# Performance work log

Hardware: AMD Instinct MI355X
Metric: run time of the kernel (lower is better)

## Reference

```python
import jax, jax.numpy as jnp
import numpy as np

N, E, B, H, DE, L, V, NB, MAXNB, T, DEPTH = 30000, 60000, 256, 256, 256, 32, 40, 4, 6, 6, 4
PT, PA, PB = 1536, 1280, 2560


def mlp2(x, w1, b1, w2, b2):
    return jax.nn.relu(x @ w1 + b1) @ w2 + b2


def setup_inputs() -> dict:
    key = jax.random.key(0)
    ks = iter(jax.random.split(key, 64))
    nrm = lambda shape, s: jax.random.normal(next(ks), shape, jnp.float32) * s
    ri = lambda shape, hi: jax.random.randint(next(ks), shape, 0, hi, dtype=jnp.int32)
    zeros = lambda shape: jnp.zeros(shape, jnp.float32)
    inp = {}
    inp["src_graph_vecs"] = nrm((B, L), 1.0)
    inp["fnode"] = nrm((N, DE), 1.0)
    inp["fmess"] = nrm((E, DE), 1.0)
    # message-passing encoder params (GraphEncoder/rnn_cell surrogate)
    inp["W_h"] = nrm((DE, H), 0.05)
    inp["U_h"] = nrm((H, H), 0.05)
    inp["b_h"] = zeros((H,))
    inp["W_o"] = nrm((DE + H, H), 0.05)
    inp["b_o"] = zeros((H,))
    # topoNN: Linear(2H+L,H) ReLU Linear(H,1)
    inp["topo_w1"] = nrm((2 * H + L, H), 0.05); inp["topo_b1"] = zeros((H,))
    inp["topo_w2"] = nrm((H, 1), 0.05); inp["topo_b2"] = zeros((1,))
    # atomNN: Linear(2H+L,H) ReLU Linear(H,V)
    inp["atom_w1"] = nrm((2 * H + L, H), 0.05); inp["atom_b1"] = zeros((H,))
    inp["atom_w2"] = nrm((H, V), 0.05); inp["atom_b2"] = zeros((V,))
    # bondNN: Linear(3H+L,H) ReLU Linear(H,NB)
    inp["bond_w1"] = nrm((3 * H + L, H), 0.05); inp["bond_b1"] = zeros((H,))
    inp["bond_w2"] = nrm((H, NB), 0.05); inp["bond_b2"] = zeros((NB,))
    # R_bond: Linear(H+V,H)+ReLU ; W_bond: Linear(H+NB,H)+ReLU
    inp["rbond_w"] = nrm((H + V, H), 0.05); inp["rbond_b"] = zeros((H,))
    inp["wbond_w"] = nrm((H + NB, H), 0.05); inp["wbond_b"] = zeros((H,))
    # graph connectivity (padded neighbor lists; index 0 = padding message)
    inp["agraph"] = ri((N, MAXNB), E)
    inp["bgraph"] = ri((E, MAXNB), E)
    inp["node2graph"] = jnp.sort(ri((N,), B))
    inp["emask_steps"] = ri((T, E), 2)
    inp["vmask_steps"] = ri((T, N), 2)
    # flattened prediction lists (topo / atom / bond)
    inp["topo_step"] = ri((PT,), T); inp["topo_bid"] = ri((PT,), B)
    inp["topo_xid"] = ri((PT,), N); inp["topo_label"] = ri((PT,), 2)
    inp["atom_step"] = ri((PA,), T); inp["atom_bid"] = ri((PA,), B)
    inp["atom_xid"] = ri((PA,), N); inp["atom_label"] = ri((PA,), V)
    # bond preds come in groups of 2 sharing step/bid; hist accumulates within a group
    G = PB // 2
    inp["bond_step"] = jnp.repeat(ri((G,), T), 2)
    inp["bond_bid"] = jnp.repeat(ri((G,), B), 2)
    inp["bond_zid"] = ri((PB,), N)
    inp["bond_atom_type"] = ri((PB,), V)
    inp["bond_label"] = ri((PB,), NB)
    inp["bond_group_start"] = (jnp.arange(PB, dtype=jnp.int32) // 2) * 2
    return inp


def reference(src_graph_vecs, fnode, fmess, W_h, U_h, b_h, W_o, b_o,
              topo_w1, topo_b1, topo_w2, topo_b2,
              atom_w1, atom_b1, atom_w2, atom_b2,
              bond_w1, bond_b1, bond_w2, bond_b2,
              rbond_w, rbond_b, wbond_w, wbond_b,
              agraph, bgraph, node2graph, emask_steps, vmask_steps,
              topo_step, topo_bid, topo_xid, topo_label,
              atom_step, atom_bid, atom_xid, atom_label,
              bond_step, bond_bid, bond_zid, bond_atom_type, bond_label,
              bond_group_start):
    pad = (jnp.arange(E) > 0).astype(fmess.dtype)[:, None]  # message 0 is padding
    pre = fmess @ W_h  # [E,H], reused across steps/depth

    def encode(em, vm):
        # apply_graph_mask: zero out not-yet-revealed message indices
        ag = agraph * em[agraph]
        bg = bgraph * em[bgraph]
        h = jnp.zeros((E, H), fmess.dtype)
        for _ in range(DEPTH):
            nei = h[bg].sum(1)                         # [E,H] gather+sum over neighbors
            h = jax.nn.relu(pre + nei @ U_h + b_h) * pad
        node = jax.nn.relu(jnp.concatenate([fnode, h[ag].sum(1)], -1) @ W_o + b_o)
        return node * vm[:, None].astype(node.dtype)

    def step(c, ms):
        em, vm = ms
        return c, encode(em, vm)

    _, nodes = jax.lax.scan(step, 0, (emask_steps, vmask_steps))  # [T,N,H]
    gvec = jax.vmap(lambda n: jax.ops.segment_sum(n, node2graph, num_segments=B))(nodes)  # [T,B,H]

    E_a = jnp.eye(V, dtype=fnode.dtype)
    E_bm = jnp.eye(NB, dtype=fnode.dtype)

    # topo: BCEWithLogits (sum)
    tv = jnp.concatenate([gvec[topo_step, topo_bid], nodes[topo_step, topo_xid],
                          src_graph_vecs[topo_bid]], -1)
    tl = mlp2(tv, topo_w1, topo_b1, topo_w2, topo_b2)[:, 0]
    ty = topo_label.astype(tl.dtype)
    topo_loss = jnp.sum(jax.nn.softplus(tl) - tl * ty)

    # atom: CrossEntropy (sum)
    av = jnp.concatenate([gvec[atom_step, atom_bid], nodes[atom_step, atom_xid],
                          src_graph_vecs[atom_bid]], -1)
    al = mlp2(av, atom_w1, atom_b1, atom_w2, atom_b2)
    atom_loss = -jnp.sum(jnp.take_along_axis(jax.nn.log_softmax(al, -1), atom_label[:, None], 1))

    # bond: hist = within-group exclusive prefix sum of W_bond(node[z], onehot(bt)), only bt>0
    zn = nodes[bond_step, bond_zid]  # [PB,H]
    wb = jax.nn.relu(jnp.concatenate([zn, E_bm[bond_label]], -1) @ wbond_w + wbond_b)
    wb = wb * (bond_label > 0).astype(wb.dtype)[:, None]
    csum = jnp.cumsum(wb, 0)
    excl = csum - wb
    hist = excl - excl[bond_group_start]
    cur = jax.nn.relu(jnp.concatenate([hist, E_a[bond_atom_type]], -1) @ rbond_w + rbond_b)
    bv = jnp.concatenate([gvec[bond_step, bond_bid], cur, zn, src_graph_vecs[bond_bid]], -1)
    bl = mlp2(bv, bond_w1, bond_b1, bond_w2, bond_b2)
    bond_loss = -jnp.sum(jnp.take_along_axis(jax.nn.log_softmax(bl, -1), bond_label[:, None], 1))

    return (topo_loss + atom_loss + bond_loss) / B
```

## Files before the change

kernel.cpp:

```cpp
#include <hip/hip_runtime.h>
#include <cstdint>
#include <cstddef>

using short8  = __attribute__((ext_vector_type(8))) short;
using floatx4 = __attribute__((ext_vector_type(4))) float;
typedef unsigned short u16;

constexpr int NN = 30000;
constexpr int NE = 60000;
constexpr int BATCH = 256;
constexpr int VV = 40;
constexpr int NBOND = 4;
constexpr int TT = 6;
constexpr int PT = 1536, PA = 1280, PB = 2560;
constexpr int PALL = PT + PA + PB;

__device__ __forceinline__ float b2f(u16 h) {
  union { unsigned u; float f; } v; v.u = ((unsigned)h) << 16; return v.f;
}
__device__ __forceinline__ u16 f2b(float f) {
  union { float f; unsigned u; } v; v.f = f;
  unsigned r = v.u + 0x7FFFu + ((v.u >> 16) & 1u);
  return (u16)(r >> 16);
}
__device__ __forceinline__ float lo16(unsigned u) {
  union { unsigned x; float f; } v; v.x = u << 16; return v.f;
}
__device__ __forceinline__ float hi16(unsigned u) {
  union { unsigned x; float f; } v; v.x = u & 0xffff0000u; return v.f;
}
__device__ __forceinline__ unsigned pack2(float a, float b) {
  return ((unsigned)f2b(a)) | (((unsigned)f2b(b)) << 16);
}

template<int AMODE>
__global__ __launch_bounds__(512) void gemm_n256_kernel(
    const void* __restrict__ Av, int M,
    const u16* __restrict__ Bt,
    u16* __restrict__ C, const float* __restrict__ abias)
{
  __shared__ __align__(16) u16 As[128][40];
  __shared__ __align__(16) u16 Bs[256][40];
  const int tid = threadIdx.x;
  const int rowbase = blockIdx.x * 128;
  const int wave = tid >> 6, lane = tid & 63;
  const int wm = wave >> 2, wn = wave & 3;
  const int lr = lane & 15, lk = (lane >> 4) * 8;
  const int arow = tid >> 2, ac8 = (tid & 3) * 8;
  const int brow = tid >> 1, bc16 = (tid & 1) * 16;

  floatx4 acc[4][4];
#pragma unroll
  for (int i = 0; i < 4; i++)
#pragma unroll
    for (int j = 0; j < 4; j++) acc[i][j] = {0.f, 0.f, 0.f, 0.f};

  for (int k0 = 0; k0 < 256; k0 += 32) {
    {
      int grow = rowbase + arow;
      uint4 av = {0u, 0u, 0u, 0u};
      if (AMODE == 1) {
        if (grow < M) {
          const float* Af = (const float*)Av;
          float4 f0 = *(const float4*)(Af + (long)grow * 256 + k0 + ac8);
          float4 f1 = *(const float4*)(Af + (long)grow * 256 + k0 + ac8 + 4);
          av.x = pack2(f0.x, f0.y); av.y = pack2(f0.z, f0.w);
          av.z = pack2(f1.x, f1.y); av.w = pack2(f1.z, f1.w);
        }
      } else {
        if (grow < M) av = *(const uint4*)((const u16*)Av + (long)grow * 256 + k0 + ac8);
        if (AMODE == 2) {
          if (grow == 0) { av = {0u, 0u, 0u, 0u}; }
          else {
            float4 b0 = *(const float4*)(abias + k0 + ac8);
            float4 b1 = *(const float4*)(abias + k0 + ac8 + 4);
            float a0 = fmaxf(lo16(av.x) + b0.x, 0.f), a1 = fmaxf(hi16(av.x) + b0.y, 0.f);
            float a2 = fmaxf(lo16(av.y) + b0.z, 0.f), a3 = fmaxf(hi16(av.y) + b0.w, 0.f);
            float a4 = fmaxf(lo16(av.z) + b1.x, 0.f), a5 = fmaxf(hi16(av.z) + b1.y, 0.f);
            float a6 = fmaxf(lo16(av.w) + b1.z, 0.f), a7 = fmaxf(hi16(av.w) + b1.w, 0.f);
            av.x = pack2(a0, a1); av.y = pack2(a2, a3);
            av.z = pack2(a4, a5); av.w = pack2(a6, a7);
          }
        }
      }
      *(uint4*)(&As[arow][ac8]) = av;
      uint4 v0 = *(const uint4*)(Bt + (long)brow * 256 + k0 + bc16);
      uint4 v1 = *(const uint4*)(Bt + (long)brow * 256 + k0 + bc16 + 8);
      *(uint4*)(&Bs[brow][bc16]) = v0;
      *(uint4*)(&Bs[brow][bc16 + 8]) = v1;
    }
    __syncthreads();
    short8 af[4], bf[4];
#pragma unroll
    for (int mt = 0; mt < 4; mt++) af[mt] = *(const short8*)(&As[wm * 64 + mt * 16 + lr][lk]);
#pragma unroll
    for (int nt = 0; nt < 4; nt++) bf[nt] = *(const short8*)(&Bs[wn * 64 + nt * 16 + lr][lk]);
#pragma unroll
    for (int mt = 0; mt < 4; mt++)
#pragma unroll
      for (int nt = 0; nt < 4; nt++)
        acc[mt][nt] = __builtin_amdgcn_mfma_f32_16x16x32_bf16(af[mt], bf[nt], acc[mt][nt], 0, 0, 0);
    __syncthreads();
  }

  const int rq = (lane >> 4) * 4;
#pragma unroll
  for (int mt = 0; mt < 4; mt++) {
#pragma unroll
    for (int nt = 0; nt < 4; nt++) {
      int gcol = wn * 64 + nt * 16 + lr;
#pragma unroll
      for (int r2 = 0; r2 < 4; r2++) {
        int grow = rowbase + wm * 64 + mt * 16 + rq + r2;
        if (grow < M) C[(long)grow * 256 + gcol] = f2b(acc[mt][nt][r2]);
      }
    }
  }
}

template<int MODE>
__global__ __launch_bounds__(256) void gemm_bt_kernel(
    const u16* __restrict__ A, int lda, int M,
    const u16* __restrict__ Bt, int K,
    u16* __restrict__ C, int ldc, const float* __restrict__ bias)
{
  __shared__ __align__(16) u16 As[128][56];
  __shared__ __align__(16) u16 Bs[128][56];
  const int tid  = threadIdx.x;
  const int wave = tid >> 6, lane = tid & 63;
  const int wm = wave >> 1, wn = wave & 1;
  const int lr = lane & 15, lk = (lane >> 4) * 8;
  const int rowbase = blockIdx.x * 128;
  const int colbase = blockIdx.y * 128;

  floatx4 acc[4][4];
#pragma unroll
  for (int i = 0; i < 4; i++)
#pragma unroll
    for (int j = 0; j < 4; j++) acc[i][j] = {0.f, 0.f, 0.f, 0.f};

  for (int k0 = 0; k0 < K; k0 += 32) {
#pragma unroll
    for (int r = 0; r < 2; r++) {
      int c = tid + 256 * r;
      int row = c >> 2, cc = (c & 3) * 8;
      int grow = rowbase + row;
      uint4 av = {0u, 0u, 0u, 0u};
      if (grow < M) av = *(const uint4*)(A + (long)grow * lda + k0 + cc);
      *(uint4*)(&As[row][cc]) = av;
      uint4 bv = *(const uint4*)(Bt + (long)(colbase + row) * K + k0 + cc);
      *(uint4*)(&Bs[row][cc]) = bv;
    }
    __syncthreads();
    short8 af[4], bf[4];
#pragma unroll
    for (int mt = 0; mt < 4; mt++) af[mt] = *(const short8*)(&As[wm * 64 + mt * 16 + lr][lk]);
#pragma unroll
    for (int nt = 0; nt < 4; nt++) bf[nt] = *(const short8*)(&Bs[wn * 64 + nt * 16 + lr][lk]);
#pragma unroll
    for (int mt = 0; mt < 4; mt++)
#pragma unroll
      for (int nt = 0; nt < 4; nt++)
        acc[mt][nt] = __builtin_amdgcn_mfma_f32_16x16x32_bf16(af[mt], bf[nt], acc[mt][nt], 0, 0, 0);
    __syncthreads();
  }

  const int rq = (lane >> 4) * 4;
#pragma unroll
  for (int mt = 0; mt < 4; mt++) {
#pragma unroll
    for (int nt = 0; nt < 4; nt++) {
      int gcol = colbase + wn * 64 + nt * 16 + lr;
#pragma unroll
      for (int r2 = 0; r2 < 4; r2++) {
        int grow = rowbase + wm * 64 + mt * 16 + rq + r2;
        if (grow < M) {
          float v = acc[mt][nt][r2];
          if (MODE == 1) { v += bias[gcol]; v = v > 0.f ? v : 0.f; }
          C[(long)grow * ldc + gcol] = f2b(v);
        }
      }
    }
  }
}

__global__ __launch_bounds__(256) void gemm_ta_kernel(
    const u16* __restrict__ A,
    const u16* __restrict__ Bt1, const u16* __restrict__ Bt2,
    const float* __restrict__ b1, const float* __restrict__ b2,
    u16* __restrict__ C)
{
  constexpr int K = 544;
  __shared__ __align__(16) u16 As[128][56];
  __shared__ __align__(16) u16 Bs[128][56];
  const int tid  = threadIdx.x;
  const int wave = tid >> 6, lane = tid & 63;
  const int wm = wave >> 1, wn = wave & 1;
  const int lr = lane & 15, lk = (lane >> 4) * 8;
  const int rowbase = blockIdx.x * 128;
  const int colbase = blockIdx.y * 128;
  const u16* Bt = (rowbase < PT) ? Bt1 : Bt2;
  const float* bias = (rowbase < PT) ? b1 : b2;

  floatx4 acc[4][4];
#pragma unroll
  for (int i = 0; i < 4; i++)
#pragma unroll
    for (int j = 0; j < 4; j++) acc[i][j] = {0.f, 0.f, 0.f, 0.f};

  for (int k0 = 0; k0 < K; k0 += 32) {
#pragma unroll
    for (int r = 0; r < 2; r++) {
      int c = tid + 256 * r;
      int row = c >> 2, cc = (c & 3) * 8;
      int grow = rowbase + row;
      uint4 av = *(const uint4*)(A + (long)grow * K + k0 + cc);
      *(uint4*)(&As[row][cc]) = av;
      uint4 bv = *(const uint4*)(Bt + (long)(colbase + row) * K + k0 + cc);
      *(uint4*)(&Bs[row][cc]) = bv;
    }
    __syncthreads();
    short8 af[4], bf[4];
#pragma unroll
    for (int mt = 0; mt < 4; mt++) af[mt] = *(const short8*)(&As[wm * 64 + mt * 16 + lr][lk]);
#pragma unroll
    for (int nt = 0; nt < 4; nt++) bf[nt] = *(const short8*)(&Bs[wn * 64 + nt * 16 + lr][lk]);
#pragma unroll
    for (int mt = 0; mt < 4; mt++)
#pragma unroll
      for (int nt = 0; nt < 4; nt++)
        acc[mt][nt] = __builtin_amdgcn_mfma_f32_16x16x32_bf16(af[mt], bf[nt], acc[mt][nt], 0, 0, 0);
    __syncthreads();
  }

  const int rq = (lane >> 4) * 4;
#pragma unroll
  for (int mt = 0; mt < 4; mt++) {
#pragma unroll
    for (int nt = 0; nt < 4; nt++) {
      int gcol = colbase + wn * 64 + nt * 16 + lr;
#pragma unroll
      for (int r2 = 0; r2 < 4; r2++) {
        int grow = rowbase + wm * 64 + mt * 16 + rq + r2;
        float v = acc[mt][nt][r2] + bias[gcol];
        v = v > 0.f ? v : 0.f;
        C[(long)grow * 256 + gcol] = f2b(v);
      }
    }
  }
}

__global__ __launch_bounds__(256) void gemm_logits_kernel(
    const u16* __restrict__ A, const u16* __restrict__ w2c,
    const float* __restrict__ b2c, float* __restrict__ L)
{
  __shared__ __align__(16) u16 As[128][40];
  __shared__ __align__(16) u16 Bs[64][40];
  const int tid = threadIdx.x;
  const int rowbase = blockIdx.x * 128;
  const int seg = (rowbase < PT) ? 0 : (rowbase < PT + PA ? 1 : 2);
  const u16* Bt = w2c + seg * 64 * 256;
  const int wave = tid >> 6, lane = tid & 63;
  const int wm = wave >> 1, wn = wave & 1;
  const int lr = lane & 15, lk = (lane >> 4) * 8;
  const int sr = tid >> 2, sc = (tid & 3) * 8;

  floatx4 acc[4][2];
#pragma unroll
  for (int i = 0; i < 4; i++)
#pragma unroll
    for (int j = 0; j < 2; j++) acc[i][j] = {0.f, 0.f, 0.f, 0.f};

  for (int k0 = 0; k0 < 256; k0 += 32) {
    *(uint4*)(&As[sr][sc]) = *(const uint4*)(A + (long)(rowbase + sr) * 256 + k0 + sc);
    *(uint4*)(&As[sr + 64][sc]) = *(const uint4*)(A + (long)(rowbase + sr + 64) * 256 + k0 + sc);
    *(uint4*)(&Bs[sr][sc]) = *(const uint4*)(Bt + (long)sr * 256 + k0 + sc);
    __syncthreads();
    short8 af[4], bf[2];
#pragma unroll
    for (int mt = 0; mt < 4; mt++) af[mt] = *(const short8*)(&As[wm * 64 + mt * 16 + lr][lk]);
#pragma unroll
    for (int nt = 0; nt < 2; nt++) bf[nt] = *(const short8*)(&Bs[wn * 32 + nt * 16 + lr][lk]);
#pragma unroll
    for (int mt = 0; mt < 4; mt++)
#pragma unroll
      for (int nt = 0; nt < 2; nt++)
        acc[mt][nt] = __builtin_amdgcn_mfma_f32_16x16x32_bf16(af[mt], bf[nt], acc[mt][nt], 0, 0, 0);
    __syncthreads();
  }

  const int rq = (lane >> 4) * 4;
#pragma unroll
  for (int mt = 0; mt < 4; mt++) {
#pragma unroll
    for (int nt = 0; nt < 2; nt++) {
      int gcol = wn * 32 + nt * 16 + lr;
#pragma unroll
      for (int r2 = 0; r2 < 4; r2++) {
        int grow = rowbase + wm * 64 + mt * 16 + rq + r2;
        L[(long)grow * 64 + gcol] = acc[mt][nt][r2] + b2c[seg * 64 + gcol];
      }
    }
  }
}

__global__ __launch_bounds__(256) void build_w2c_kernel(
    const float* __restrict__ tw2, const float* __restrict__ tb2,
    const float* __restrict__ aw2, const float* __restrict__ ab2,
    const float* __restrict__ bw2, const float* __restrict__ bb2,
    u16* __restrict__ w2c, float* __restrict__ b2c)
{
  int idx = blockIdx.x * 256 + threadIdx.x;
  int seg = idx / 16384;
  int rem = idx - seg * 16384;
  int n = rem >> 8, k = rem & 255;
  const float* W; const float* B; int NC;
  if (seg == 0)      { W = tw2; B = tb2; NC = 1; }
  else if (seg == 1) { W = aw2; B = ab2; NC = VV; }
  else               { W = bw2; B = bb2; NC = NBOND; }
  w2c[idx] = (n < NC) ? f2b(W[(long)k * NC + n]) : (u16)0;
  if (idx < 192) {
    int s2 = idx / 64, n2 = idx & 63;
    const float* B2 = (s2 == 0) ? tb2 : (s2 == 1 ? ab2 : bb2);
    int NC2 = (s2 == 0) ? 1 : (s2 == 1 ? VV : NBOND);
    b2c[idx] = (n2 < NC2) ? B2[n2] : 0.f;
  }
}

__global__ __launch_bounds__(256) void loss_finalize_kernel(
    const float* __restrict__ L,
    const int* __restrict__ tlab, const int* __restrict__ alab,
    const int* __restrict__ blab, float* __restrict__ out)
{
  __shared__ float part[4];
  int wave = threadIdx.x >> 6, lane = threadIdx.x & 63;
  int r = blockIdx.x * 4 + wave;
  float contrib = 0.f;
  if (r < PT) {
    float l = L[(long)r * 64];
    float y = (float)tlab[r];
    contrib = fmaxf(l, 0.f) + log1pf(expf(-fabsf(l))) - l * y;
  } else {
    int NC, lb;
    if (r < PT + PA) { NC = VV; lb = alab[r - PT]; }
    else             { NC = NBOND; lb = blab[r - PT - PA]; }
    bool valid = lane < NC;
    float logit = valid ? L[(long)r * 64 + lane] : -1e30f;
    float m = logit;
#pragma unroll
    for (int off = 32; off > 0; off >>= 1) m = fmaxf(m, __shfl_xor(m, off));
    float e = valid ? expf(logit - m) : 0.f;
#pragma unroll
    for (int off = 32; off > 0; off >>= 1) e += __shfl_xor(e, off);
    float lse = m + logf(e);
    float ll = __shfl(logit, lb);
    contrib = lse - ll;
  }
  if (lane == 0) part[wave] = contrib;
  __syncthreads();
  if (threadIdx.x == 0)
    atomicAdd(out, (part[0] + part[1] + part[2] + part[3]) * (1.0f / BATCH));
}

template<int SHARED_TAB>
__global__ __launch_bounds__(256) void gather_e2_kernel(
    const u16* __restrict__ tab, const u16* __restrict__ pre,
    const int* __restrict__ bgraph, const int* __restrict__ emask,
    const float* __restrict__ bias, int t0, u16* __restrict__ G)
{
  int r0 = blockIdx.x * 8;
  int tl = r0 / NE;
  int e0 = r0 - tl * NE;
  const int* em_t = emask + (long)(t0 + tl) * NE;
  __shared__ int sidx[8][6];
  int tid = threadIdx.x;
  if (tid < 48) {
    int rr = tid / 6, j = tid - rr * 6;
    int v = bgraph[(long)(e0 + rr) * 6 + j];
    v = v * em_t[v];
    sidx[rr][j] = SHARED_TAB ? v : (tl * NE + v);
  }
  __syncthreads();
  int rl = tid >> 5, ch = (tid & 31) * 8;
  int e = e0 + rl;
  uint4 p = *(const uint4*)(pre + (long)e * 256 + ch);
  float a0 = lo16(p.x), a1 = hi16(p.x), a2 = lo16(p.y), a3 = hi16(p.y);
  float a4 = lo16(p.z), a5 = hi16(p.z), a6 = lo16(p.w), a7 = hi16(p.w);
#pragma unroll
  for (int j = 0; j < 6; j++) {
    uint4 g = *(const uint4*)(tab + (long)sidx[rl][j] * 256 + ch);
    a0 += lo16(g.x); a1 += hi16(g.x); a2 += lo16(g.y); a3 += hi16(g.y);
    a4 += lo16(g.z); a5 += hi16(g.z); a6 += lo16(g.w); a7 += hi16(g.w);
  }
  float4 b0 = *(const float4*)(bias + ch);
  float4 b1 = *(const float4*)(bias + ch + 4);
  a0 += b0.x; a1 += b0.y; a2 += b0.z; a3 += b0.w;
  a4 += b1.x; a5 += b1.y; a6 += b1.z; a7 += b1.w;
  if (e == 0) { a0 = a1 = a2 = a3 = a4 = a5 = a6 = a7 = 0.f; }
  else {
    a0 = fmaxf(a0, 0.f); a1 = fmaxf(a1, 0.f); a2 = fmaxf(a2, 0.f); a3 = fmaxf(a3, 0.f);
    a4 = fmaxf(a4, 0.f); a5 = fmaxf(a5, 0.f); a6 = fmaxf(a6, 0.f); a7 = fmaxf(a7, 0.f);
  }
  uint4 o; o.x = pack2(a0, a1); o.y = pack2(a2, a3); o.z = pack2(a4, a5); o.w = pack2(a6, a7);
  *(uint4*)(G + (long)(r0 + rl) * 256 + ch) = o;
}

__global__ __launch_bounds__(256) void gather_n2_kernel(
    const u16* __restrict__ tab, const u16* __restrict__ fo,
    const int* __restrict__ agraph, const int* __restrict__ emask,
    const float* __restrict__ bias, const int* __restrict__ vmask,
    int t0, u16* __restrict__ node)
{
  int r0 = blockIdx.x * 8;
  int tl = r0 / NN;
  int n0 = r0 - tl * NN;
  const int* em_t = emask + (long)(t0 + tl) * NE;
  const int* vm_t = vmask + (long)(t0 + tl) * NN;
  __shared__ int sidx[8][6];
  __shared__ int svm[8];
  int tid = threadIdx.x;
  if (tid < 48) {
    int rr = tid / 6, j = tid - rr * 6;
    int v = agraph[(long)(n0 + rr) * 6 + j];
    sidx[rr][j] = tl * NE + v * em_t[v];
  }
  if (tid >= 48 && tid < 56) svm[tid - 48] = vm_t[n0 + (tid - 48)];
  __syncthreads();
  int rl = tid >> 5, ch = (tid & 31) * 8;
  int n = n0 + rl;
  uint4 p = *(const uint4*)(fo + (long)n * 256 + ch);
  float a0 = lo16(p.x), a1 = hi16(p.x), a2 = lo16(p.y), a3 = hi16(p.y);
  float a4 = lo16(p.z), a5 = hi16(p.z), a6 = lo16(p.w), a7 = hi16(p.w);
#pragma unroll
  for (int j = 0; j < 6; j++) {
    uint4 g = *(const uint4*)(tab + (long)sidx[rl][j] * 256 + ch);
    a0 += lo16(g.x); a1 += hi16(g.x); a2 += lo16(g.y); a3 += hi16(g.y);
    a4 += lo16(g.z); a5 += hi16(g.z); a6 += lo16(g.w); a7 += hi16(g.w);
  }
  float4 b0 = *(const float4*)(bias + ch);
  float4 b1 = *(const float4*)(bias + ch + 4);
  a0 = fmaxf(a0 + b0.x, 0.f); a1 = fmaxf(a1 + b0.y, 0.f);
  a2 = fmaxf(a2 + b0.z, 0.f); a3 = fmaxf(a3 + b0.w, 0.f);
  a4 = fmaxf(a4 + b1.x, 0.f); a5 = fmaxf(a5 + b1.y, 0.f);
  a6 = fmaxf(a6 + b1.z, 0.f); a7 = fmaxf(a7 + b1.w, 0.f);
  if (svm[rl] == 0) { a0 = a1 = a2 = a3 = a4 = a5 = a6 = a7 = 0.f; }
  uint4 o; o.x = pack2(a0, a1); o.y = pack2(a2, a3); o.z = pack2(a4, a5); o.w = pack2(a6, a7);
  *(uint4*)(node + (long)(r0 + rl) * 256 + ch) = o;
}

__global__ __launch_bounds__(256) void init_zero_kernel(float* __restrict__ gv,
                                                        float* __restrict__ out)
{
  int i = blockIdx.x * 256 + threadIdx.x;
  gv[i] = 0.f;
  if (i == 0) out[0] = 0.f;
}

__global__ __launch_bounds__(256) void transpose_all_kernel(
    const float* W_h, const float* U_h, const float* W_o,
    const float* tw1, const float* aw1, const float* bw1,
    const float* rw, const float* ww,
    u16* Wh_t, u16* Uh_t, u16* Wo1_t, u16* Wo2_t,
    u16* tw1_t, u16* aw1_t, u16* bw1_t, u16* rw_t, u16* ww_t)
{
  int b = blockIdx.x;
  const float* W; int K, Kpad; u16* Bt; int base;
  if      (b < 256)  { W = W_h;  K = 256; Kpad = 256; Bt = Wh_t;  base = 0; }
  else if (b < 512)  { W = U_h;  K = 256; Kpad = 256; Bt = Uh_t;  base = 256; }
  else if (b < 768)  { W = W_o;  K = 256; Kpad = 256; Bt = Wo1_t; base = 512; }
  else if (b < 1024) { W = W_o + 256 * 256; K = 256; Kpad = 256; Bt = Wo2_t; base = 768; }
  else if (b < 1568) { W = tw1;  K = 544; Kpad = 544; Bt = tw1_t; base = 1024; }
  else if (b < 2112) { W = aw1;  K = 544; Kpad = 544; Bt = aw1_t; base = 1568; }
  else if (b < 2912) { W = bw1;  K = 800; Kpad = 800; Bt = bw1_t; base = 2112; }
  else if (b < 3232) { W = rw;   K = 296; Kpad = 320; Bt = rw_t;  base = 2912; }
  else               { W = ww;   K = 260; Kpad = 288; Bt = ww_t;  base = 3232; }
  int idx = (b - base) * 256 + threadIdx.x;
  int n = idx / Kpad, k = idx - n * Kpad;
  Bt[idx] = (k < K) ? f2b(W[(long)k * 256 + n]) : (u16)0;
}

__global__ __launch_bounds__(256) void gvec_head_kernel(int t0,
    const u16* __restrict__ node, const int* __restrict__ n2g,
    float* __restrict__ gv,
    const int* __restrict__ tstep, const int* __restrict__ txid,
    const int* __restrict__ astep, const int* __restrict__ axid,
    const int* __restrict__ bstep, const int* __restrict__ bzid,
    u16* __restrict__ tv, u16* __restrict__ av, u16* __restrict__ bv,
    u16* __restrict__ wbin)
{
  int b = blockIdx.x;
  if (b < 1876) {
    int tl = (b >= 938) ? 1 : 0;
    int r0 = (b - tl * 938) * 32;
    if (r0 >= NN) return;
    int h = threadIdx.x;
    const u16* nd = node + (long)tl * NN * 256;
    float* gb = gv + (long)(t0 + tl) * BATCH * 256;
    int rend = r0 + 32; if (rend > NN) rend = NN;
    int gprev = n2g[r0];
    float acc = 0.f;
    for (int r = r0; r < rend; r++) {
      int g = n2g[r];
      if (g != gprev) { atomicAdd(gb + gprev * 256 + h, acc); acc = 0.f; gprev = g; }
      acc += b2f(nd[(long)r * 256 + h]);
    }
    atomicAdd(gb + gprev * 256 + h, acc);
    return;
  }
  int wave = threadIdx.x >> 6, lane = threadIdx.x & 63;
  int r = (b - 1876) * 4 + wave;
  int c = lane * 4;
  if (r < PT) {
    int st = tstep[r];
    if (st < t0 || st >= t0 + 2) return;
    ushort4 v = *(const ushort4*)(node + ((long)(st - t0) * NN + txid[r]) * 256 + c);
    *(ushort4*)(tv + (long)r * 544 + 256 + c) = v;
  } else if (r < PT + PA) {
    int i = r - PT;
    int st = astep[i];
    if (st < t0 || st >= t0 + 2) return;
    ushort4 v = *(const ushort4*)(node + ((long)(st - t0) * NN + axid[i]) * 256 + c);
    *(ushort4*)(av + (long)i * 544 + 256 + c) = v;
  } else if (r < PALL) {
    int i = r - PT - PA;
    int st = bstep[i];
    if (st < t0 || st >= t0 + 2) return;
    ushort4 v = *(const ushort4*)(node + ((long)(st - t0) * NN + bzid[i]) * 256 + c);
    *(ushort4*)(bv + (long)i * 800 + 512 + c) = v;
    *(ushort4*)(wbin + (long)i * 288 + c) = v;
  }
}

__global__ __launch_bounds__(256) void build_static_kernel(
    const float* __restrict__ gvec, const float* __restrict__ src,
    const int* __restrict__ tstep, const int* __restrict__ tbid,
    const int* __restrict__ astep, const int* __restrict__ abid,
    const int* __restrict__ bstep, const int* __restrict__ bbid,
    const int* __restrict__ blabel, const int* __restrict__ batype,
    u16* __restrict__ tv, u16* __restrict__ av, u16* __restrict__ bv,
    u16* __restrict__ wbin, u16* __restrict__ rbin)
{
  int wave = threadIdx.x >> 6, lane = threadIdx.x & 63;
  int r = blockIdx.x * 4 + wave;
  int c = lane * 4;
  if (r < PT) {
    int st = tstep[r], bid = tbid[r];
    const float* g = gvec + ((long)st * BATCH + bid) * 256;
    u16* d = tv + (long)r * 544;
    float4 g4 = *(const float4*)(g + c);
    d[c] = f2b(g4.x); d[c + 1] = f2b(g4.y); d[c + 2] = f2b(g4.z); d[c + 3] = f2b(g4.w);
    if (lane < 8) {
      float4 s4 = *(const float4*)(src + bid * 32 + c);
      d[512 + c] = f2b(s4.x); d[512 + c + 1] = f2b(s4.y);
      d[512 + c + 2] = f2b(s4.z); d[512 + c + 3] = f2b(s4.w);
    }
  } else if (r < PT + PA) {
    int i = r - PT;
    int st = astep[i], bid = abid[i];
    const float* g = gvec + ((long)st * BATCH + bid) * 256;
    u16* d = av + (long)i * 544;
    float4 g4 = *(const float4*)(g + c);
    d[c] = f2b(g4.x); d[c + 1] = f2b(g4.y); d[c + 2] = f2b(g4.z); d[c + 3] = f2b(g4.w);
    if (lane < 8) {
      float4 s4 = *(const float4*)(src + bid * 32 + c);
      d[512 + c] = f2b(s4.x); d[512 + c + 1] = f2b(s4.y);
      d[512 + c + 2] = f2b(s4.z); d[512 + c + 3] = f2b(s4.w);
    }
  } else if (r < PALL) {
    int i = r - PT - PA;
    int st = bstep[i], bid = bbid[i];
    const float* g = gvec + ((long)st * BATCH + bid) * 256;
    u16* d = bv + (long)i * 800;
    float4 g4 = *(const float4*)(g + c);
    d[c] = f2b(g4.x); d[c + 1] = f2b(g4.y); d[c + 2] = f2b(g4.z); d[c + 3] = f2b(g4.w);
    if (lane < 8) {
      float4 s4 = *(const float4*)(src + bid * 32 + c);
      d[768 + c] = f2b(s4.x); d[768 + c + 1] = f2b(s4.y);
      d[768 + c + 2] = f2b(s4.z); d[768 + c + 3] = f2b(s4.w);
      int bl = blabel[i];
      u16* wd = wbin + (long)i * 288 + 256;
      for (int q = 0; q < 4; q++) {
        int k = c + q;
        wd[k] = f2b((k < NBOND && bl == k) ? 1.f : 0.f);
      }
    }
    if (lane < 16) {
      int at = batype[i];
      u16* rd = rbin + (long)i * 320 + 256;
      for (int q = 0; q < 4; q++) {
        int k = c + q;
        rd[k] = f2b((k < VV && at == k) ? 1.f : 0.f);
      }
    }
  }
}

__global__ __launch_bounds__(256) void hist_kernel(
    const u16* __restrict__ wb, const int* __restrict__ gs_arr,
    const int* __restrict__ blabel, u16* __restrict__ rbin)
{
  int wave = threadIdx.x >> 6, lane = threadIdx.x & 63;
  int r = blockIdx.x * 4 + wave;
  if (r >= PB) return;
  int c = lane * 4;
  float a0 = 0.f, a1 = 0.f, a2 = 0.f, a3 = 0.f;
  int gs = gs_arr[r];
  for (int j = gs; j < r; j++) {
    if (blabel[j] > 0) {
      ushort4 g = *(const ushort4*)(wb + (long)j * 256 + c);
      a0 += b2f(g.x); a1 += b2f(g.y); a2 += b2f(g.z); a3 += b2f(g.w);
    }
  }
  u16* rd = rbin + (long)r * 320;
  rd[c] = f2b(a0); rd[c + 1] = f2b(a1); rd[c + 2] = f2b(a2); rd[c + 3] = f2b(a3);
}

extern "C" void kernel_launch(void* const* d_in, const int* in_sizes, int n_in,
                              void* d_out, int out_size, void* d_ws, size_t ws_size,
                              hipStream_t stream)
{
  const float* src      = (const float*)d_in[0];
  const float* fnode    = (const float*)d_in[1];
  const float* fmess    = (const float*)d_in[2];
  const float* W_h      = (const float*)d_in[3];
  const float* U_h      = (const float*)d_in[4];
  const float* b_h      = (const float*)d_in[5];
  const float* W_o      = (const float*)d_in[6];
  const float* b_o      = (const float*)d_in[7];
  const float* topo_w1  = (const float*)d_in[8];
  const float* topo_b1  = (const float*)d_in[9];
  const float* topo_w2  = (const float*)d_in[10];
  const float* topo_b2  = (const float*)d_in[11];
  const float* atom_w1  = (const float*)d_in[12];
  const float* atom_b1  = (const float*)d_in[13];
  const float* atom_w2  = (const float*)d_in[14];
  const float* atom_b2  = (const float*)d_in[15];
  const float* bond_w1  = (const float*)d_in[16];
  const float* bond_b1  = (const float*)d_in[17];
  const float* bond_w2  = (const float*)d_in[18];
  const float* bond_b2  = (const float*)d_in[19];
  const float* rbond_w  = (const float*)d_in[20];
  const float* rbond_b  = (const float*)d_in[21];
  const float* wbond_w  = (const float*)d_in[22];
  const float* wbond_b  = (const float*)d_in[23];
  const int* agraph     = (const int*)d_in[24];
  const int* bgraph     = (const int*)d_in[25];
  const int* node2graph = (const int*)d_in[26];
  const int* emask      = (const int*)d_in[27];
  const int* vmask      = (const int*)d_in[28];
  const int* topo_step  = (const int*)d_in[29];
  const int* topo_bid   = (const int*)d_in[30];
  const int* topo_xid   = (const int*)d_in[31];
  const int* topo_label = (const int*)d_in[32];
  const int* atom_step  = (const int*)d_in[33];
  const int* atom_bid   = (const int*)d_in[34];
  const int* atom_xid   = (const int*)d_in[35];
  const int* atom_label = (const int*)d_in[36];
  const int* bond_step  = (const int*)d_in[37];
  const int* bond_bid   = (const int*)d_in[38];
  const int* bond_zid   = (const int*)d_in[39];
  const int* bond_atype = (const int*)d_in[40];
  const int* bond_label = (const int*)d_in[41];
  const int* bond_gs    = (const int*)d_in[42];

  char* wp = (char*)d_ws;
  auto alloc = [&](size_t bytes) -> char* {
    char* p = wp; wp += (bytes + 255) & ~(size_t)255; return p;
  };
  u16* preB    = (u16*)alloc((size_t)NE * 256 * 2);
  u16* hu1B    = (u16*)alloc((size_t)NE * 256 * 2);
  u16* foB     = (u16*)alloc((size_t)NN * 256 * 2);
  float* gvec  = (float*)alloc((size_t)TT * BATCH * 256 * 4);
  u16* Wh_t    = (u16*)alloc(256 * 256 * 2);
  u16* Uh_t    = (u16*)alloc(256 * 256 * 2);
  u16* Wo1_t   = (u16*)alloc(256 * 256 * 2);
  u16* Wo2_t   = (u16*)alloc(256 * 256 * 2);
  u16* tw1_t   = (u16*)alloc(256 * 544 * 2);
  u16* aw1_t   = (u16*)alloc(256 * 544 * 2);
  u16* bw1_t   = (u16*)alloc(256 * 800 * 2);
  u16* rw_t    = (u16*)alloc(256 * 320 * 2);
  u16* ww_t    = (u16*)alloc(256 * 288 * 2);
  u16* w2c     = (u16*)alloc(3 * 64 * 256 * 2);
  float* b2c   = (float*)alloc(192 * 4);
  u16* tva     = (u16*)alloc((size_t)(PT + PA) * 544 * 2);
  u16* bv      = (u16*)alloc((size_t)PB * 800 * 2);
  u16* wbin    = (u16*)alloc((size_t)PB * 288 * 2);
  u16* rbin    = (u16*)alloc((size_t)PB * 320 * 2);
  u16* wb      = (u16*)alloc((size_t)PB * 256 * 2);
  u16* hid_all = (u16*)alloc((size_t)PALL * 256 * 2);
  float* logitsL = (float*)alloc((size_t)PALL * 64 * 4);
  u16* G       = (u16*)alloc((size_t)2 * NE * 256 * 2);
  u16* T       = (u16*)alloc((size_t)2 * NE * 256 * 2);
  u16* tv      = tva;
  u16* av      = tva + (size_t)PT * 544;
  u16* nodeB   = G;

  float* out = (float*)d_out;

  init_zero_kernel<<<1536, 256, 0, stream>>>(gvec, out);
  transpose_all_kernel<<<3520, 256, 0, stream>>>(W_h, U_h, W_o, topo_w1, atom_w1, bond_w1,
      rbond_w, wbond_w, Wh_t, Uh_t, Wo1_t, Wo2_t, tw1_t, aw1_t, bw1_t, rw_t, ww_t);
  build_w2c_kernel<<<192, 256, 0, stream>>>(topo_w2, topo_b2, atom_w2, atom_b2,
                                            bond_w2, bond_b2, w2c, b2c);

  gemm_n256_kernel<1><<<(NE + 127) / 128, 512, 0, stream>>>(fmess, NE, Wh_t, preB, nullptr);
  gemm_n256_kernel<1><<<(NN + 127) / 128, 512, 0, stream>>>(fnode, NN, Wo1_t, foB, nullptr);
  gemm_n256_kernel<2><<<(NE + 127) / 128, 512, 0, stream>>>(preB, NE, Uh_t, hu1B, b_h);

  for (int t0 = 0; t0 < TT; t0 += 2) {
    int M2 = 2 * NE;
    int gb = 2 * NE / 8;
    int mb = (M2 + 127) / 128;
    gather_e2_kernel<1><<<gb, 256, 0, stream>>>(hu1B, preB, bgraph, emask, b_h, t0, G);
    gemm_n256_kernel<0><<<mb, 512, 0, stream>>>(G, M2, Uh_t, T, nullptr);
    gather_e2_kernel<0><<<gb, 256, 0, stream>>>(T, preB, bgraph, emask, b_h, t0, G);
    gemm_n256_kernel<0><<<mb, 512, 0, stream>>>(G, M2, Uh_t, T, nullptr);
    gather_e2_kernel<0><<<gb, 256, 0, stream>>>(T, preB, bgraph, emask, b_h, t0, G);
    gemm_n256_kernel<0><<<mb, 512, 0, stream>>>(G, M2, Wo2_t, T, nullptr);
    gather_n2_kernel<<<2 * NN / 8, 256, 0, stream>>>(T, foB, agraph, emask, b_o,
                                                     vmask, t0, nodeB);
    gvec_head_kernel<<<3220, 256, 0, stream>>>(t0, nodeB, node2graph, gvec,
        topo_step, topo_xid, atom_step, atom_xid, bond_step, bond_zid,
        tv, av, bv, wbin);
  }

  build_static_kernel<<<1344, 256, 0, stream>>>(gvec, src,
      topo_step, topo_bid, atom_step, atom_bid, bond_step, bond_bid,
      bond_label, bond_atype, tv, av, bv, wbin, rbin);

  gemm_ta_kernel<<<dim3((PT + PA) / 128, 2), 256, 0, stream>>>(tva, tw1_t, aw1_t,
                                                               topo_b1, atom_b1, hid_all);
  gemm_bt_kernel<1><<<dim3(20, 2), 256, 0, stream>>>(wbin, 288, PB, ww_t, 288,
                                                     wb, 256, wbond_b);
  hist_kernel<<<640, 256, 0, stream>>>(wb, bond_gs, bond_label, rbin);
  gemm_bt_kernel<1><<<dim3(20, 2), 256, 0, stream>>>(rbin, 320, PB, rw_t, 320,
                                                     bv + 256, 800, rbond_b);
  gemm_bt_kernel<1><<<dim3(20, 2), 256, 0, stream>>>(bv, 800, PB, bw1_t, 800,
                                                     hid_all + (size_t)(PT + PA) * 256,
                                                     256, bond_b1);

  gemm_logits_kernel<<<PALL / 128, 256, 0, stream>>>(hid_all, w2c, b2c, logitsL);
  loss_finalize_kernel<<<PALL / 4, 256, 0, stream>>>(logitsL, topo_label, atom_label,
                                                     bond_label, out);
}
```

Baseline: 1.140 ms.

## Store message-passing intermediates in FP8 to halve gather and GEMM traffic

The edge message tensors (pre-activations, hidden updates, gather outputs and GEMM outputs in the recurrent loop) are stored as FP8 bytes instead of bf16, with conversion to bf16 when loading GEMM A tiles and FP8 packing on output. This halves the memory traffic of the bandwidth-bound gather and GEMM passes over 120k-row buffers. nodeB gets its own buffer since G shrank. The trade-off is a large loss of precision in the recurrent message state, which may push the loss outside tolerance.

```diff
diff --git a/kernel.cpp b/kernel.cpp
--- a/kernel.cpp
+++ b/kernel.cpp
@@ -4,7 +4,9 @@
 
 using short8  = __attribute__((ext_vector_type(8))) short;
 using floatx4 = __attribute__((ext_vector_type(4))) float;
+using floatx2 = __attribute__((ext_vector_type(2))) float;
 typedef unsigned short u16;
+typedef unsigned char  u8;
 
 constexpr int NN = 30000;
 constexpr int NE = 60000;
@@ -32,12 +34,26 @@
 __device__ __forceinline__ unsigned pack2(float a, float b) {
   return ((unsigned)f2b(a)) | (((unsigned)f2b(b)) << 16);
 }
-
-template<int AMODE>
+__device__ __forceinline__ floatx2 f8lo(unsigned v) {
+  return __builtin_amdgcn_cvt_pk_f32_fp8((int)v, false);
+}
+__device__ __forceinline__ floatx2 f8hi(unsigned v) {
+  return __builtin_amdgcn_cvt_pk_f32_fp8((int)v, true);
+}
+__device__ __forceinline__ unsigned pk8(float a, float b, float c, float d) {
+  int w = __builtin_amdgcn_cvt_pk_fp8_f32(a, b, 0, false);
+  w = __builtin_amdgcn_cvt_pk_fp8_f32(c, d, w, true);
+  return (unsigned)w;
+}
+__device__ __forceinline__ u8 f2f8(float v) {
+  return (u8)(__builtin_amdgcn_cvt_pk_fp8_f32(v, v, 0, false) & 0xff);
+}
+
+template<int AMODE, int OMODE>
 __global__ __launch_bounds__(512) void gemm_n256_kernel(
     const void* __restrict__ Av, int M,
     const u16* __restrict__ Bt,
-    u16* __restrict__ C, const float* __restrict__ abias)
+    void* __restrict__ Cv, const float* __restrict__ abias)
 {
   __shared__ __align__(16) u16 As[128][40];
   __shared__ __align__(16) u16 Bs[256][40];
@@ -68,19 +84,25 @@
           av.z = pack2(f1.x, f1.y); av.w = pack2(f1.z, f1.w);
         }
       } else {
-        if (grow < M) av = *(const uint4*)((const u16*)Av + (long)grow * 256 + k0 + ac8);
-        if (AMODE == 2) {
-          if (grow == 0) { av = {0u, 0u, 0u, 0u}; }
-          else {
-            float4 b0 = *(const float4*)(abias + k0 + ac8);
-            float4 b1 = *(const float4*)(abias + k0 + ac8 + 4);
-            float a0 = fmaxf(lo16(av.x) + b0.x, 0.f), a1 = fmaxf(hi16(av.x) + b0.y, 0.f);
-            float a2 = fmaxf(lo16(av.y) + b0.z, 0.f), a3 = fmaxf(hi16(av.y) + b0.w, 0.f);
-            float a4 = fmaxf(lo16(av.z) + b1.x, 0.f), a5 = fmaxf(hi16(av.z) + b1.y, 0.f);
-            float a6 = fmaxf(lo16(av.w) + b1.z, 0.f), a7 = fmaxf(hi16(av.w) + b1.w, 0.f);
-            av.x = pack2(a0, a1); av.y = pack2(a2, a3);
-            av.z = pack2(a4, a5); av.w = pack2(a6, a7);
+        if (grow < M) {
+          const u8* Af8 = (const u8*)Av;
+          uint2 v8 = *(const uint2*)(Af8 + (long)grow * 256 + k0 + ac8);
+          floatx2 f0 = f8lo(v8.x), f1 = f8hi(v8.x), f2 = f8lo(v8.y), f3 = f8hi(v8.y);
+          float a0 = f0.x, a1 = f0.y, a2 = f1.x, a3 = f1.y;
+          float a4 = f2.x, a5 = f2.y, a6 = f3.x, a7 = f3.y;
+          if (AMODE == 2) {
+            if (grow == 0) { a0 = a1 = a2 = a3 = a4 = a5 = a6 = a7 = 0.f; }
+            else {
+              float4 b0 = *(const float4*)(abias + k0 + ac8);
+              float4 b1 = *(const float4*)(abias + k0 + ac8 + 4);
+              a0 = fmaxf(a0 + b0.x, 0.f); a1 = fmaxf(a1 + b0.y, 0.f);
+              a2 = fmaxf(a2 + b0.z, 0.f); a3 = fmaxf(a3 + b0.w, 0.f);
+              a4 = fmaxf(a4 + b1.x, 0.f); a5 = fmaxf(a5 + b1.y, 0.f);
+              a6 = fmaxf(a6 + b1.z, 0.f); a7 = fmaxf(a7 + b1.w, 0.f);
+            }
           }
+          av.x = pack2(a0, a1); av.y = pack2(a2, a3);
+          av.z = pack2(a4, a5); av.w = pack2(a6, a7);
         }
       }
       *(uint4*)(&As[arow][ac8]) = av;
@@ -112,7 +134,11 @@
 #pragma unroll
       for (int r2 = 0; r2 < 4; r2++) {
         int grow = rowbase + wm * 64 + mt * 16 + rq + r2;
-        if (grow < M) C[(long)grow * 256 + gcol] = f2b(acc[mt][nt][r2]);
+        if (grow < M) {
+          float v = acc[mt][nt][r2];
+          if (OMODE == 0) ((u16*)Cv)[(long)grow * 256 + gcol] = f2b(v);
+          else            ((u8*)Cv)[(long)grow * 256 + gcol] = f2f8(v);
+        }
       }
     }
   }
@@ -314,10 +340,10 @@
   int seg = idx / 16384;
   int rem = idx - seg * 16384;
   int n = rem >> 8, k = rem & 255;
-  const float* W; const float* B; int NC;
-  if (seg == 0)      { W = tw2; B = tb2; NC = 1; }
-  else if (seg == 1) { W = aw2; B = ab2; NC = VV; }
-  else               { W = bw2; B = bb2; NC = NBOND; }
+  const float* W; int NC;
+  if (seg == 0)      { W = tw2; NC = 1; }
+  else if (seg == 1) { W = aw2; NC = VV; }
+  else               { W = bw2; NC = NBOND; }
   w2c[idx] = (n < NC) ? f2b(W[(long)k * NC + n]) : (u16)0;
   if (idx < 192) {
     int s2 = idx / 64, n2 = idx & 63;
@@ -364,9 +390,9 @@
 
 template<int SHARED_TAB>
 __global__ __launch_bounds__(256) void gather_e2_kernel(
-    const u16* __restrict__ tab, const u16* __restrict__ pre,
+    const u8* __restrict__ tab, const u8* __restrict__ pre,
     const int* __restrict__ bgraph, const int* __restrict__ emask,
-    const float* __restrict__ bias, int t0, u16* __restrict__ G)
+    const float* __restrict__ bias, int t0, u8* __restrict__ G)
 {
   int r0 = blockIdx.x * 8;
   int tl = r0 / NE;
@@ -383,14 +409,16 @@
   __syncthreads();
   int rl = tid >> 5, ch = (tid & 31) * 8;
   int e = e0 + rl;
-  uint4 p = *(const uint4*)(pre + (long)e * 256 + ch);
-  float a0 = lo16(p.x), a1 = hi16(p.x), a2 = lo16(p.y), a3 = hi16(p.y);
-  float a4 = lo16(p.z), a5 = hi16(p.z), a6 = lo16(p.w), a7 = hi16(p.w);
+  uint2 p = *(const uint2*)(pre + (long)e * 256 + ch);
+  floatx2 p0 = f8lo(p.x), p1 = f8hi(p.x), p2 = f8lo(p.y), p3 = f8hi(p.y);
+  float a0 = p0.x, a1 = p0.y, a2 = p1.x, a3 = p1.y;
+  float a4 = p2.x, a5 = p2.y, a6 = p3.x, a7 = p3.y;
 #pragma unroll
   for (int j = 0; j < 6; j++) {
-    uint4 g = *(const uint4*)(tab + (long)sidx[rl][j] * 256 + ch);
-    a0 += lo16(g.x); a1 += hi16(g.x); a2 += lo16(g.y); a3 += hi16(g.y);
-    a4 += lo16(g.z); a5 += hi16(g.z); a6 += lo16(g.w); a7 += hi16(g.w);
+    uint2 g = *(const uint2*)(tab + (long)sidx[rl][j] * 256 + ch);
+    floatx2 g0 = f8lo(g.x), g1 = f8hi(g.x), g2 = f8lo(g.y), g3 = f8hi(g.y);
+    a0 += g0.x; a1 += g0.y; a2 += g1.x; a3 += g1.y;
+    a4 += g2.x; a5 += g2.y; a6 += g3.x; a7 += g3.y;
   }
   float4 b0 = *(const float4*)(bias + ch);
   float4 b1 = *(const float4*)(bias + ch + 4);
@@ -401,12 +429,12 @@
     a0 = fmaxf(a0, 0.f); a1 = fmaxf(a1, 0.f); a2 = fmaxf(a2, 0.f); a3 = fmaxf(a3, 0.f);
     a4 = fmaxf(a4, 0.f); a5 = fmaxf(a5, 0.f); a6 = fmaxf(a6, 0.f); a7 = fmaxf(a7, 0.f);
   }
-  uint4 o; o.x = pack2(a0, a1); o.y = pack2(a2, a3); o.z = pack2(a4, a5); o.w = pack2(a6, a7);
-  *(uint4*)(G + (long)(r0 + rl) * 256 + ch) = o;
+  uint2 o; o.x = pk8(a0, a1, a2, a3); o.y = pk8(a4, a5, a6, a7);
+  *(uint2*)(G + (long)(r0 + rl) * 256 + ch) = o;
 }
 
 __global__ __launch_bounds__(256) void gather_n2_kernel(
-    const u16* __restrict__ tab, const u16* __restrict__ fo,
+    const u8* __restrict__ tab, const u16* __restrict__ fo,
     const int* __restrict__ agraph, const int* __restrict__ emask,
     const float* __restrict__ bias, const int* __restrict__ vmask,
     int t0, u16* __restrict__ node)
@@ -433,9 +461,10 @@
   float a4 = lo16(p.z), a5 = hi16(p.z), a6 = lo16(p.w), a7 = hi16(p.w);
 #pragma unroll
   for (int j = 0; j < 6; j++) {
-    uint4 g = *(const uint4*)(tab + (long)sidx[rl][j] * 256 + ch);
-    a0 += lo16(g.x); a1 += hi16(g.x); a2 += lo16(g.y); a3 += hi16(g.y);
-    a4 += lo16(g.z); a5 += hi16(g.z); a6 += lo16(g.w); a7 += hi16(g.w);
+    uint2 g = *(const uint2*)(tab + (long)sidx[rl][j] * 256 + ch);
+    floatx2 g0 = f8lo(g.x), g1 = f8hi(g.x), g2 = f8lo(g.y), g3 = f8hi(g.y);
+    a0 += g0.x; a1 += g0.y; a2 += g1.x; a3 += g1.y;
+    a4 += g2.x; a5 += g2.y; a6 += g3.x; a7 += g3.y;
   }
   float4 b0 = *(const float4*)(bias + ch);
   float4 b1 = *(const float4*)(bias + ch + 4);
@@ -667,8 +696,8 @@
   auto alloc = [&](size_t bytes) -> char* {
     char* p = wp; wp += (bytes + 255) & ~(size_t)255; return p;
   };
-  u16* preB    = (u16*)alloc((size_t)NE * 256 * 2);
-  u16* hu1B    = (u16*)alloc((size_t)NE * 256 * 2);
+  u8*  preB    = (u8*)alloc((size_t)NE * 256);
+  u8*  hu1B    = (u8*)alloc((size_t)NE * 256);
   u16* foB     = (u16*)alloc((size_t)NN * 256 * 2);
   float* gvec  = (float*)alloc((size_t)TT * BATCH * 256 * 4);
   u16* Wh_t    = (u16*)alloc(256 * 256 * 2);
@@ -689,11 +718,11 @@
   u16* wb      = (u16*)alloc((size_t)PB * 256 * 2);
   u16* hid_all = (u16*)alloc((size_t)PALL * 256 * 2);
   float* logitsL = (float*)alloc((size_t)PALL * 64 * 4);
-  u16* G       = (u16*)alloc((size_t)2 * NE * 256 * 2);
-  u16* T       = (u16*)alloc((size_t)2 * NE * 256 * 2);
+  u8*  G       = (u8*)alloc((size_t)2 * NE * 256);
+  u8*  T       = (u8*)alloc((size_t)2 * NE * 256);
+  u16* nodeB   = (u16*)alloc((size_t)2 * NN * 256 * 2);
   u16* tv      = tva;
   u16* av      = tva + (size_t)PT * 544;
-  u16* nodeB   = G;
 
   float* out = (float*)d_out;
 
@@ -703,20 +732,23 @@
   build_w2c_kernel<<<192, 256, 0, stream>>>(topo_w2, topo_b2, atom_w2, atom_b2,
                                             bond_w2, bond_b2, w2c, b2c);
 
-  gemm_n256_kernel<1><<<(NE + 127) / 128, 512, 0, stream>>>(fmess, NE, Wh_t, preB, nullptr);
-  gemm_n256_kernel<1><<<(NN + 127) / 128, 512, 0, stream>>>(fnode, NN, Wo1_t, foB, nullptr);
-  gemm_n256_kernel<2><<<(NE + 127) / 128, 512, 0, stream>>>(preB, NE, Uh_t, hu1B, b_h);
+  gemm_n256_kernel<1, 1><<<(NE + 127) / 128, 512, 0, stream>>>(
+      fmess, NE, Wh_t, preB, nullptr);
+  gemm_n256_kernel<1, 0><<<(NN + 127) / 128, 512, 0, stream>>>(
+      fnode, NN, Wo1_t, foB, nullptr);
+  gemm_n256_kernel<2, 1><<<(NE + 127) / 128, 512, 0, stream>>>(
+      preB, NE, Uh_t, hu1B, b_h);
 
   for (int t0 = 0; t0 < TT; t0 += 2) {
     int M2 = 2 * NE;
     int gb = 2 * NE / 8;
     int mb = (M2 + 127) / 128;
     gather_e2_kernel<1><<<gb, 256, 0, stream>>>(hu1B, preB, bgraph, emask, b_h, t0, G);
-    gemm_n256_kernel<0><<<mb, 512, 0, stream>>>(G, M2, Uh_t, T, nullptr);
+    gemm_n256_kernel<3, 1><<<mb, 512, 0, stream>>>(G, M2, Uh_t, T, nullptr);
     gather_e2_kernel<0><<<gb, 256, 0, stream>>>(T, preB, bgraph, emask, b_h, t0, G);
-    gemm_n256_kernel<0><<<mb, 512, 0, stream>>>(G, M2, Uh_t, T, nullptr);
+    gemm_n256_kernel<3, 1><<<mb, 512, 0, stream>>>(G, M2, Uh_t, T, nullptr);
     gather_e2_kernel<0><<<gb, 256, 0, stream>>>(T, preB, bgraph, emask, b_h, t0, G);
-    gemm_n256_kernel<0><<<mb, 512, 0, stream>>>(G, M2, Wo2_t, T, nullptr);
+    gemm_n256_kernel<3, 1><<<mb, 512, 0, stream>>>(G, M2, Wo2_t, T, nullptr);
     gather_n2_kernel<<<2 * NN / 8, 256, 0, stream>>>(T, foB, agraph, emask, b_o,
                                                      vmask, t0, nodeB);
     gvec_head_kernel<<<3220, 256, 0, stream>>>(t0, nodeB, node2graph, gvec,
```

Result: faster. 973.9 us (-14.6%).
